# Kernel optimization log

Measured on AMD Instinct MI355X. Metric: run time of the kernel, lower is better.

The kernel has to match this reference:

```python
import jax, jax.numpy as jnp
from jax import lax
import numpy as np

NPOINT, RADIUS, NSAMPLE = 1024, 0.2, 32
MLP = [64, 64, 128]
IN_CH = 35  # 3 coord channels + 32 point features
EPS = 1e-5


def farthest_point_sample(xyz, npoint):
    # xyz: (B, N, 3) -> (B, npoint) int32. Deterministic start at index 0.
    B, N, _ = xyz.shape

    def step(carry, _):
        dist, farthest = carry  # (B,N), (B,)
        centroid = jnp.take_along_axis(xyz, farthest[:, None, None], axis=1)  # (B,1,3)
        d = jnp.sum((xyz - centroid) ** 2, axis=-1)  # (B,N)
        dist = jnp.minimum(dist, d)
        nxt = jnp.argmax(dist, axis=-1).astype(jnp.int32)
        return (dist, nxt), farthest

    init = (jnp.full((B, N), 1e10, xyz.dtype), jnp.zeros((B,), jnp.int32))
    _, idxs = lax.scan(step, init, None, length=npoint)
    return idxs.T  # (B, npoint)


def gather_points(points, idx):
    # points: (B, N, C); idx: (B, ...) int -> (B, ..., C)
    return jax.vmap(lambda p, i: p[i])(points, idx)


def query_ball_point(radius, nsample, xyz, new_xyz):
    # xyz: (B,N,3), new_xyz: (B,S,3) -> (B,S,nsample) int32
    B, N, _ = xyz.shape
    sqrdists = jnp.sum((new_xyz[:, :, None, :] - xyz[:, None, :, :]) ** 2, axis=-1)  # (B,S,N)
    group_idx = jnp.where(sqrdists > radius ** 2, N, jnp.arange(N, dtype=jnp.int32))
    group_idx = jnp.sort(group_idx, axis=-1)[:, :, :nsample]
    first = group_idx[:, :, :1]
    return jnp.where(group_idx == N, first, group_idx)


def sa_forward(xyz, points, params):
    B, N, C = xyz.shape
    fps_idx = farthest_point_sample(xyz, NPOINT)
    new_xyz = gather_points(xyz, fps_idx)  # (B,S,3)
    idx = query_ball_point(RADIUS, NSAMPLE, xyz, new_xyz)  # (B,S,K)
    grouped_xyz = gather_points(xyz, idx)  # (B,S,K,3)
    grouped_xyz_norm = grouped_xyz - new_xyz[:, :, None, :]
    grouped_points = gather_points(points, idx)  # (B,S,K,D)
    new_points = jnp.concatenate([grouped_xyz_norm, grouped_points], axis=-1)  # (B,S,K,Cin)
    x = new_points.transpose(0, 3, 2, 1)  # (B, Cin, K, S)
    for w, b, g, be in params:
        x = jnp.einsum('oi,biks->boks', w, x) + b[None, :, None, None]  # 1x1 conv
        mean = x.mean(axis=(0, 2, 3), keepdims=True)  # BatchNorm2d, training mode
        var = x.var(axis=(0, 2, 3), keepdims=True)
        x = (x - mean) / jnp.sqrt(var + EPS)
        x = jax.nn.relu(g[None, :, None, None] * x + be[None, :, None, None])
    new_points_out = x.max(axis=2)  # max over nsample -> (B, Cout, S)
    return new_xyz, new_points_out


def setup_inputs() -> dict:
    key = jax.random.key(0)
    ks = jax.random.split(key, 16)
    B, N, D = 16, 4096, 32
    inp = {
        'xyz': jax.random.uniform(ks[0], (B, N, 3), dtype=jnp.float32),
        'points': jax.random.normal(ks[1], (B, N, D), dtype=jnp.float32),
    }
    last = IN_CH
    for li, out_ch in enumerate(MLP):
        inp[f'w{li}'] = jax.random.normal(ks[2 + 4 * li], (out_ch, last), dtype=jnp.float32) * 0.05
        inp[f'b{li}'] = jnp.zeros((out_ch,), jnp.float32)
        inp[f'g{li}'] = jnp.ones((out_ch,), jnp.float32)
        inp[f'be{li}'] = jnp.zeros((out_ch,), jnp.float32)
        last = out_ch
    return inp


def reference(xyz, points, w0, b0, g0, be0, w1, b1, g1, be1, w2, b2, g2, be2):
    params = [(w0, b0, g0, be0), (w1, b1, g1, be1), (w2, b2, g2, be2)]
    return sa_forward(xyz, points, params)
```

## Files before the change

kernel.cpp:

```cpp
#include <hip/hip_runtime.h>
#include <stdint.h>

#pragma clang fp contract(off)

#define BATCH   16
#define NPTS    4096
#define NPOINT  1024
#define NSAMPLE 32
#define NPOS    (BATCH*NPOINT*NSAMPLE)
#define NBLK    (NPOS/128)
#define EPSV    1e-5f

typedef unsigned short ushort_t;
typedef unsigned int uint_t;
typedef unsigned long long u64;
typedef __attribute__((ext_vector_type(8))) short bf16x8;
typedef __attribute__((ext_vector_type(4))) float f32x4;
typedef __attribute__((ext_vector_type(2))) float f32x2;

__device__ inline ushort_t f2bf(float f) {
    uint_t u = __float_as_uint(f);
    u += 0x7fffu + ((u >> 16) & 1u);
    return (ushort_t)(u >> 16);
}
__device__ inline void unpack8(uint4 u, float* f) {
    f[0] = __uint_as_float(u.x << 16); f[1] = __uint_as_float(u.x & 0xffff0000u);
    f[2] = __uint_as_float(u.y << 16); f[3] = __uint_as_float(u.y & 0xffff0000u);
    f[4] = __uint_as_float(u.z << 16); f[5] = __uint_as_float(u.z & 0xffff0000u);
    f[6] = __uint_as_float(u.w << 16); f[7] = __uint_as_float(u.w & 0xffff0000u);
}

#define DPP_MAX_STAGE(CTRL) do {                                              \
    uint_t _lo2 = __builtin_amdgcn_update_dpp(lo, lo, CTRL, 0xf, 0xf, false); \
    uint_t _hi2 = __builtin_amdgcn_update_dpp(hi, hi, CTRL, 0xf, 0xf, false); \
    u64 _o = ((u64)_hi2 << 32) | _lo2;                                        \
    u64 _v = ((u64)hi << 32) | lo;                                            \
    bool _g = _o > _v;                                                        \
    lo = _g ? _lo2 : lo; hi = _g ? _hi2 : hi;                                 \
} while (0)

__global__ __launch_bounds__(512) void fps_kernel(const float* __restrict__ xyz,
                                                  float* __restrict__ new_xyz) {
    __shared__ float4 lxyz[NPTS];
    __shared__ u64 wbest[2][8];
    __shared__ int fpsidx[NPOINT];
    const int b = blockIdx.x;
    const int tid = threadIdx.x;
    const float* base = xyz + (size_t)b * NPTS * 3;
    for (int n = tid; n < NPTS; n += 512) {
        lxyz[n] = make_float4(base[3 * n], base[3 * n + 1], base[3 * n + 2], 0.f);
    }
    __syncthreads();

    f32x2 px[4], py[4], pz[4], dist[4];
    uint_t lowc[8];
#pragma unroll
    for (int j = 0; j < 4; j++) {
        float4 v0 = lxyz[tid + (2 * j) * 512];
        float4 v1 = lxyz[tid + (2 * j + 1) * 512];
        px[j] = (f32x2){v0.x, v1.x};
        py[j] = (f32x2){v0.y, v1.y};
        pz[j] = (f32x2){v0.z, v1.z};
        dist[j] = (f32x2){1e10f, 1e10f};
        lowc[2 * j] = ~(uint_t)(tid + (2 * j) * 512);
        lowc[2 * j + 1] = ~(uint_t)(tid + (2 * j + 1) * 512);
    }
    if (tid == 0) fpsidx[0] = 0;
    int cur = 0;
    const int lane = tid & 63, wid = tid >> 6;

    for (int it = 1; it < NPOINT; ++it) {
        float4 c = lxyz[cur];
        const f32x2 cx = (f32x2){c.x, c.x};
        const f32x2 cy = (f32x2){c.y, c.y};
        const f32x2 cz = (f32x2){c.z, c.z};
        u64 t[4];
#pragma unroll
        for (int j = 0; j < 4; j++) {
            f32x2 dx = px[j] - cx;
            f32x2 dy = py[j] - cy;
            f32x2 dz = pz[j] - cz;
            f32x2 d = (dx * dx + dy * dy) + dz * dz;
            f32x2 nd = __builtin_elementwise_min(dist[j], d);
            dist[j] = nd;
            u64 e0 = ((u64)__float_as_uint(nd.x) << 32) | lowc[2 * j];
            u64 e1 = ((u64)__float_as_uint(nd.y) << 32) | lowc[2 * j + 1];
            t[j] = e0 > e1 ? e0 : e1;
        }
        t[0] = t[0] > t[1] ? t[0] : t[1];
        t[2] = t[2] > t[3] ? t[2] : t[3];
        u64 v = t[0] > t[2] ? t[0] : t[2];

        uint_t lo = (uint_t)v, hi = (uint_t)(v >> 32);
        DPP_MAX_STAGE(0x111);
        DPP_MAX_STAGE(0x112);
        DPP_MAX_STAGE(0x114);
        DPP_MAX_STAGE(0x118);
        DPP_MAX_STAGE(0x142);
        DPP_MAX_STAGE(0x143);
        uint_t mlo = __builtin_amdgcn_readlane(lo, 63);
        uint_t mhi = __builtin_amdgcn_readlane(hi, 63);

        const int par = it & 1;
        if (lane == 0) wbest[par][wid] = ((u64)mhi << 32) | mlo;
        __syncthreads();
        u64 w0 = wbest[par][0], w1 = wbest[par][1];
        u64 w2 = wbest[par][2], w3 = wbest[par][3];
        u64 w4 = wbest[par][4], w5 = wbest[par][5];
        u64 w6 = wbest[par][6], w7 = wbest[par][7];
        u64 a0 = w0 > w1 ? w0 : w1;
        u64 a1 = w2 > w3 ? w2 : w3;
        u64 a2 = w4 > w5 ? w4 : w5;
        u64 a3 = w6 > w7 ? w6 : w7;
        a0 = a0 > a1 ? a0 : a1;
        a2 = a2 > a3 ? a2 : a3;
        u64 bb = a0 > a2 ? a0 : a2;
        cur = (int)(~(uint_t)bb) & (NPTS - 1);
        if (tid == 0) fpsidx[it] = cur;
    }
    __syncthreads();
    float* ob = new_xyz + (size_t)b * NPOINT * 3;
    for (int s = tid; s < NPOINT; s += 512) {
        float4 v = lxyz[fpsidx[s]];
        ob[3 * s + 0] = v.x; ob[3 * s + 1] = v.y; ob[3 * s + 2] = v.z;
    }
}

__global__ __launch_bounds__(256) void ballq_kernel(const float* __restrict__ xyz,
                                                    const float* __restrict__ new_xyz,
                                                    int* __restrict__ gidx) {
    const int gw = (int)((blockIdx.x * 256 + threadIdx.x) >> 6);
    const int lane = threadIdx.x & 63;
    const int b = gw / NPOINT, s = gw % NPOINT;
    const float* nb = new_xyz + ((size_t)b * NPOINT + s) * 3;
    const float cx = nb[0], cy = nb[1], cz = nb[2];
    const float* xb = xyz + (size_t)b * NPTS * 3;
    const float r2 = (float)(0.2 * 0.2);
    int cnt = 0;
    int first = -1;
    int* out = gidx + (size_t)gw * NSAMPLE;
    for (int j0 = 0; j0 < NPTS; j0 += 64) {
        int j = j0 + lane;
        float dx = __fsub_rn(xb[j * 3 + 0], cx);
        float dy = __fsub_rn(xb[j * 3 + 1], cy);
        float dz = __fsub_rn(xb[j * 3 + 2], cz);
        float d = __fadd_rn(__fadd_rn(__fmul_rn(dx, dx), __fmul_rn(dy, dy)),
                            __fmul_rn(dz, dz));
        bool pred = !(d > r2);
        u64 mask = __ballot(pred);
        if (first < 0 && mask != 0ull) first = j0 + (__ffsll((long long)mask) - 1);
        int before = __popcll(mask & ((1ull << lane) - 1ull));
        int slot = cnt + before;
        if (pred && slot < NSAMPLE) out[slot] = j;
        cnt += (int)__popcll(mask);
        if (cnt >= NSAMPLE) break;
    }
    if (cnt < NSAMPLE) {
        if (lane >= cnt && lane < NSAMPLE) out[lane] = first;
    }
}

__global__ __launch_bounds__(256) void conv1_mfma(const float* __restrict__ xyz,
                                                  const float* __restrict__ points,
                                                  const float* __restrict__ new_xyz,
                                                  const int* __restrict__ gidx,
                                                  const float* __restrict__ W,
                                                  const float* __restrict__ bias,
                                                  ushort_t* __restrict__ Y,
                                                  float* __restrict__ part_s,
                                                  float* __restrict__ part_q) {
    const int lane = threadIdx.x & 63, wid = threadIdx.x >> 6;
    const int l15 = lane & 15, quad = lane >> 4;
    const int p0 = blockIdx.x * 128 + wid * 32;

    bf16x8 Bp[4], Bx[4];
#pragma unroll
    for (int nt = 0; nt < 4; nt++) {
        const float* wr = W + (size_t)(nt * 16 + l15) * 35;
#pragma unroll
        for (int q = 0; q < 8; q++) Bp[nt][q] = (short)f2bf(wr[3 + quad * 8 + q]);
#pragma unroll
        for (int q = 0; q < 8; q++)
            Bx[nt][q] = (quad == 0 && q < 3) ? (short)f2bf(wr[q]) : (short)0;
    }
    f32x4 acc[2][4];
#pragma unroll
    for (int mt = 0; mt < 2; mt++)
#pragma unroll
        for (int nt = 0; nt < 4; nt++) acc[mt][nt] = (f32x4){0.f, 0.f, 0.f, 0.f};

#pragma unroll
    for (int mt = 0; mt < 2; mt++) {
        const int p = p0 + mt * 16 + l15;
        const int b = p >> 15, s = (p & 32767) >> 5;
        const int j = gidx[p];
        const float* pr = points + ((size_t)(b * NPTS + j)) * 32 + quad * 8;
        bf16x8 Ap, Ax;
#pragma unroll
        for (int q = 0; q < 8; q++) Ap[q] = (short)f2bf(pr[q]);
#pragma unroll
        for (int q = 0; q < 8; q++) Ax[q] = 0;
        const float* xp = xyz + ((size_t)(b * NPTS + j)) * 3;
        const float* nz = new_xyz + ((size_t)(b * NPOINT + s)) * 3;
        if (quad == 0) {
            Ax[0] = (short)f2bf(xp[0] - nz[0]);
            Ax[1] = (short)f2bf(xp[1] - nz[1]);
            Ax[2] = (short)f2bf(xp[2] - nz[2]);
        }
#pragma unroll
        for (int nt = 0; nt < 4; nt++) {
            acc[mt][nt] = __builtin_amdgcn_mfma_f32_16x16x32_bf16(Ap, Bp[nt], acc[mt][nt], 0, 0, 0);
            acc[mt][nt] = __builtin_amdgcn_mfma_f32_16x16x32_bf16(Ax, Bx[nt], acc[mt][nt], 0, 0, 0);
        }
    }
    float s_[4], q_[4];
#pragma unroll
    for (int nt = 0; nt < 4; nt++) { s_[nt] = 0.f; q_[nt] = 0.f; }
#pragma unroll
    for (int nt = 0; nt < 4; nt++) {
        const int ch = nt * 16 + l15;
        const float bs = bias[ch];
#pragma unroll
        for (int mt = 0; mt < 2; mt++) {
            const int pb = p0 + mt * 16 + quad * 4;
#pragma unroll
            for (int r = 0; r < 4; r++) {
                float x = acc[mt][nt][r] + bs;
                uint_t u = __float_as_uint(x);
                u += 0x7fffu + ((u >> 16) & 1u);
                Y[(size_t)(pb + r) * 64 + ch] = (ushort_t)(u >> 16);
                float v = __uint_as_float(u & 0xffff0000u);
                s_[nt] += v; q_[nt] += v * v;
            }
        }
    }
#pragma unroll
    for (int nt = 0; nt < 4; nt++) {
        s_[nt] += __shfl_xor(s_[nt], 16, 64); s_[nt] += __shfl_xor(s_[nt], 32, 64);
        q_[nt] += __shfl_xor(q_[nt], 16, 64); q_[nt] += __shfl_xor(q_[nt], 32, 64);
    }
    __shared__ float reds[4][4][16], redq[4][4][16];
    if (lane < 16) {
#pragma unroll
        for (int nt = 0; nt < 4; nt++) { reds[wid][nt][lane] = s_[nt]; redq[wid][nt][lane] = q_[nt]; }
    }
    __syncthreads();
    if (threadIdx.x < 16) {
#pragma unroll
        for (int nt = 0; nt < 4; nt++) {
            float ss = 0.f, qq = 0.f;
#pragma unroll
            for (int w = 0; w < 4; w++) { ss += reds[w][nt][threadIdx.x]; qq += redq[w][nt][threadIdx.x]; }
            const int ch = nt * 16 + threadIdx.x;
            part_s[(size_t)ch * NBLK + blockIdx.x] = ss;
            part_q[(size_t)ch * NBLK + blockIdx.x] = qq;
        }
    }
}

template <int IN, int OUT>
__global__ __launch_bounds__(256) void convN_mfma(const ushort_t* __restrict__ Yin,
                                                  const float* __restrict__ scale,
                                                  const float* __restrict__ shift,
                                                  const float* __restrict__ W,
                                                  const float* __restrict__ bias,
                                                  ushort_t* __restrict__ Yout,
                                                  float* __restrict__ part_s,
                                                  float* __restrict__ part_q) {
    constexpr int NT = OUT / 16;
    const int lane = threadIdx.x & 63, wid = threadIdx.x >> 6;
    const int l15 = lane & 15, quad = lane >> 4;
    const int p0 = blockIdx.x * 128 + wid * 32;

    float sc[2][8], sh[2][8];
#pragma unroll
    for (int kq = 0; kq < 2; kq++) {
        const int i0 = kq * 32 + quad * 8;
#pragma unroll
        for (int q = 0; q < 8; q++) { sc[kq][q] = scale[i0 + q]; sh[kq][q] = shift[i0 + q]; }
    }
    bf16x8 Bf[NT][2];
#pragma unroll
    for (int nt = 0; nt < NT; nt++)
#pragma unroll
        for (int kq = 0; kq < 2; kq++) {
            const float* wr = W + (size_t)(nt * 16 + l15) * IN + kq * 32 + quad * 8;
#pragma unroll
            for (int q = 0; q < 8; q++) Bf[nt][kq][q] = (short)f2bf(wr[q]);
        }

    bf16x8 Af[2][2];
#pragma unroll
    for (int mt = 0; mt < 2; mt++)
#pragma unroll
        for (int kq = 0; kq < 2; kq++) {
            const ushort_t* yr = Yin + (size_t)(p0 + mt * 16 + l15) * IN + kq * 32 + quad * 8;
            uint4 u = *(const uint4*)yr;
            float f[8]; unpack8(u, f);
#pragma unroll
            for (int q = 0; q < 8; q++) {
                float x = fmaxf(fmaf(f[q], sc[kq][q], sh[kq][q]), 0.f);
                Af[mt][kq][q] = (short)f2bf(x);
            }
        }

    f32x4 acc[2][NT];
#pragma unroll
    for (int mt = 0; mt < 2; mt++)
#pragma unroll
        for (int nt = 0; nt < NT; nt++) acc[mt][nt] = (f32x4){0.f, 0.f, 0.f, 0.f};
#pragma unroll
    for (int mt = 0; mt < 2; mt++)
#pragma unroll
        for (int nt = 0; nt < NT; nt++) {
            acc[mt][nt] = __builtin_amdgcn_mfma_f32_16x16x32_bf16(Af[mt][0], Bf[nt][0], acc[mt][nt], 0, 0, 0);
            acc[mt][nt] = __builtin_amdgcn_mfma_f32_16x16x32_bf16(Af[mt][1], Bf[nt][1], acc[mt][nt], 0, 0, 0);
        }
    float s_[NT], q_[NT];
#pragma unroll
    for (int nt = 0; nt < NT; nt++) { s_[nt] = 0.f; q_[nt] = 0.f; }
#pragma unroll
    for (int nt = 0; nt < NT; nt++) {
        const int ch = nt * 16 + l15;
        const float bs = bias[ch];
#pragma unroll
        for (int mt = 0; mt < 2; mt++) {
            const int pb = p0 + mt * 16 + quad * 4;
#pragma unroll
            for (int r = 0; r < 4; r++) {
                float x = acc[mt][nt][r] + bs;
                uint_t u = __float_as_uint(x);
                u += 0x7fffu + ((u >> 16) & 1u);
                Yout[(size_t)(pb + r) * OUT + ch] = (ushort_t)(u >> 16);
                float v = __uint_as_float(u & 0xffff0000u);
                s_[nt] += v; q_[nt] += v * v;
            }
        }
    }
#pragma unroll
    for (int nt = 0; nt < NT; nt++) {
        s_[nt] += __shfl_xor(s_[nt], 16, 64); s_[nt] += __shfl_xor(s_[nt], 32, 64);
        q_[nt] += __shfl_xor(q_[nt], 16, 64); q_[nt] += __shfl_xor(q_[nt], 32, 64);
    }
    __shared__ float reds[4][NT][16], redq[4][NT][16];
    if (lane < 16) {
#pragma unroll
        for (int nt = 0; nt < NT; nt++) { reds[wid][nt][lane] = s_[nt]; redq[wid][nt][lane] = q_[nt]; }
    }
    __syncthreads();
    if (threadIdx.x < 16) {
#pragma unroll
        for (int nt = 0; nt < NT; nt++) {
            float ss = 0.f, qq = 0.f;
#pragma unroll
            for (int w = 0; w < 4; w++) { ss += reds[w][nt][threadIdx.x]; qq += redq[w][nt][threadIdx.x]; }
            const int ch = nt * 16 + threadIdx.x;
            part_s[(size_t)ch * NBLK + blockIdx.x] = ss;
            part_q[(size_t)ch * NBLK + blockIdx.x] = qq;
        }
    }
}

__global__ __launch_bounds__(256) void reduce_finalize(const float* __restrict__ part_s,
                                                       const float* __restrict__ part_q,
                                                       const float* __restrict__ g,
                                                       const float* __restrict__ be,
                                                       float* __restrict__ scale,
                                                       float* __restrict__ shift) {
    const int ch = blockIdx.x;
    const float* p1 = part_s + (size_t)ch * NBLK;
    const float* p2 = part_q + (size_t)ch * NBLK;
    float s = 0.f, q = 0.f;
    for (int i = threadIdx.x; i < NBLK; i += 256) { s += p1[i]; q += p2[i]; }
#pragma unroll
    for (int m = 1; m < 64; m <<= 1) { s += __shfl_xor(s, m, 64); q += __shfl_xor(q, m, 64); }
    __shared__ float ls[4], lq[4];
    const int lane = threadIdx.x & 63, wid = threadIdx.x >> 6;
    if (lane == 0) { ls[wid] = s; lq[wid] = q; }
    __syncthreads();
    if (threadIdx.x == 0) {
        float ssum = ls[0] + ls[1] + ls[2] + ls[3];
        float qsum = lq[0] + lq[1] + lq[2] + lq[3];
        float mean = ssum * (1.f / (float)NPOS);
        float var = qsum * (1.f / (float)NPOS) - mean * mean;
        float inv = 1.f / sqrtf(var + EPSV);
        float sc = g[ch] * inv;
        scale[ch] = sc;
        shift[ch] = be[ch] - mean * sc;
    }
}

__global__ __launch_bounds__(256) void final_kernel(const ushort_t* __restrict__ Y3,
                                                    const float* __restrict__ scale,
                                                    const float* __restrict__ shift,
                                                    float* __restrict__ out) {
    const int b = blockIdx.x >> 5;
    const int stile = (blockIdx.x & 31) * 32;
    const int sl = threadIdx.x >> 3;
    const int oc = threadIdx.x & 7;
    const int s = stile + sl;
    const size_t base = ((size_t)(b * NPOINT + s)) * 32 * 128 + oc * 16;
    float vmax[16];
#pragma unroll
    for (int i = 0; i < 16; i++) vmax[i] = 0.f;
    for (int k = 0; k < 32; k++) {
        const ushort_t* yp = Y3 + base + (size_t)k * 128;
#pragma unroll
        for (int h = 0; h < 2; h++) {
            uint4 u = *(const uint4*)(yp + h * 8);
            float f[8];
            unpack8(u, f);
#pragma unroll
            for (int i = 0; i < 8; i++) {
                int o = oc * 16 + h * 8 + i;
                float v = fmaf(f[i], scale[o], shift[o]);
                vmax[h * 8 + i] = fmaxf(vmax[h * 8 + i], v);
            }
        }
    }
    __shared__ float res[32][130];
#pragma unroll
    for (int i = 0; i < 16; i++) res[sl][oc * 16 + i] = vmax[i];
    __syncthreads();
    const int so = threadIdx.x & 31;
    const int og = threadIdx.x >> 5;
#pragma unroll
    for (int r = 0; r < 16; r++) {
        int o = og * 16 + r;
        out[((size_t)(b * 128 + o)) * NPOINT + stile + so] = res[so][o];
    }
}

extern "C" void kernel_launch(void* const* d_in, const int* in_sizes, int n_in,
                              void* d_out, int out_size, void* d_ws, size_t ws_size,
                              hipStream_t stream) {
    const float* xyz = (const float*)d_in[0];
    const float* points = (const float*)d_in[1];
    const float* w0 = (const float*)d_in[2];
    const float* b0 = (const float*)d_in[3];
    const float* g0 = (const float*)d_in[4];
    const float* be0 = (const float*)d_in[5];
    const float* w1 = (const float*)d_in[6];
    const float* b1 = (const float*)d_in[7];
    const float* g1 = (const float*)d_in[8];
    const float* be1 = (const float*)d_in[9];
    const float* w2 = (const float*)d_in[10];
    const float* b2 = (const float*)d_in[11];
    const float* g2 = (const float*)d_in[12];
    const float* be2 = (const float*)d_in[13];

    float* out = (float*)d_out;
    float* new_xyz = out;
    float* final_out = out + BATCH * NPOINT * 3;

    char* ws = (char*)d_ws;
    const size_t MB = 1024u * 1024u;
    const size_t o_gidx = 0;
    const size_t o_y2 = 2 * MB;
    const size_t o_y13 = o_y2 + (size_t)NPOS * 64 * 2;
    const size_t o_params = o_y13 + (size_t)NPOS * 128 * 2;
    const size_t o_parts = o_params + 4096;

    int* gidx = (int*)(ws + o_gidx);
    ushort_t* Y1 = (ushort_t*)(ws + o_y13);
    ushort_t* Y2 = (ushort_t*)(ws + o_y2);
    ushort_t* Y3 = (ushort_t*)(ws + o_y13);
    float* pr = (float*)(ws + o_params);
    float* scale1 = pr + 0, *shift1 = pr + 64;
    float* scale2 = pr + 128, *shift2 = pr + 192;
    float* scale3 = pr + 256, *shift3 = pr + 384;
    float* part_s = (float*)(ws + o_parts);
    float* part_q = part_s + (size_t)128 * NBLK;

    fps_kernel<<<BATCH, 512, 0, stream>>>(xyz, new_xyz);
    ballq_kernel<<<(BATCH * NPOINT) / 4, 256, 0, stream>>>(xyz, new_xyz, gidx);
    conv1_mfma<<<NBLK, 256, 0, stream>>>(xyz, points, new_xyz, gidx, w0, b0, Y1, part_s, part_q);
    reduce_finalize<<<64, 256, 0, stream>>>(part_s, part_q, g0, be0, scale1, shift1);
    convN_mfma<64, 64><<<NBLK, 256, 0, stream>>>(Y1, scale1, shift1, w1, b1, Y2, part_s, part_q);
    reduce_finalize<<<64, 256, 0, stream>>>(part_s, part_q, g1, be1, scale2, shift2);
    convN_mfma<64, 128><<<NBLK, 256, 0, stream>>>(Y2, scale2, shift2, w2, b2, Y3, part_s, part_q);
    reduce_finalize<<<128, 256, 0, stream>>>(part_s, part_q, g2, be2, scale3, shift3);
    final_kernel<<<BATCH * 32, 256, 0, stream>>>(Y3, scale3, shift3, final_out);
}
```

Baseline: 1.048 ms.

## Pre-convert weights to bf16, halve FPS block size, pack bf16 conversions

A new prep kernel converts the conv weights to bf16 once per call, so each conv block loads them with vector loads instead of converting them itself. The FPS kernel drops from 512 to 256 threads per block, with each thread holding 16 points, which halves the cross-wave reduction at every iteration's barrier. Conv kernels switch to vector float4 loads and paired bf16 packing intrinsics for the activation conversion and the output epilogue. The costs are an extra kernel launch, more registers per FPS thread, and longer serial work per thread in FPS.

```diff
diff --git a/kernel.cpp b/kernel.cpp
--- a/kernel.cpp
+++ b/kernel.cpp
@@ -1,4 +1,5 @@
 #include <hip/hip_runtime.h>
+#include <hip/hip_bf16.h>
 #include <stdint.h>
 
 #pragma clang fp contract(off)
@@ -23,11 +24,33 @@
     u += 0x7fffu + ((u >> 16) & 1u);
     return (ushort_t)(u >> 16);
 }
+__device__ inline uint_t pkbf(float a, float b) {
+    __hip_bfloat162 h = __float22bfloat162_rn(make_float2(a, b));
+    uint_t r; __builtin_memcpy(&r, &h, 4); return r;
+}
+__device__ inline bf16x8 asbf(uint4 u) {
+    bf16x8 v; __builtin_memcpy(&v, &u, 16); return v;
+}
 __device__ inline void unpack8(uint4 u, float* f) {
     f[0] = __uint_as_float(u.x << 16); f[1] = __uint_as_float(u.x & 0xffff0000u);
     f[2] = __uint_as_float(u.y << 16); f[3] = __uint_as_float(u.y & 0xffff0000u);
     f[4] = __uint_as_float(u.z << 16); f[5] = __uint_as_float(u.z & 0xffff0000u);
     f[6] = __uint_as_float(u.w << 16); f[7] = __uint_as_float(u.w & 0xffff0000u);
+}
+
+__global__ __launch_bounds__(256) void prep_w(const float* __restrict__ w0,
+                                              const float* __restrict__ w1,
+                                              const float* __restrict__ w2,
+                                              ushort_t* __restrict__ Wp0,
+                                              ushort_t* __restrict__ Wx0,
+                                              ushort_t* __restrict__ Wp1,
+                                              ushort_t* __restrict__ Wp2) {
+    const int t = blockIdx.x * 256 + threadIdx.x;
+    const int stride = gridDim.x * 256;
+    for (int i = t; i < 64 * 32; i += stride) { int ch = i >> 5, k = i & 31; Wp0[i] = f2bf(w0[ch * 35 + 3 + k]); }
+    for (int i = t; i < 64 * 4;  i += stride) { int ch = i >> 2, q = i & 3;  Wx0[i] = (q < 3) ? f2bf(w0[ch * 35 + q]) : (ushort_t)0; }
+    for (int i = t; i < 64 * 64; i += stride) Wp1[i] = f2bf(w1[i]);
+    for (int i = t; i < 128 * 64; i += stride) Wp2[i] = f2bf(w2[i]);
 }
 
 #define DPP_MAX_STAGE(CTRL) do {                                              \
@@ -39,31 +62,31 @@
     lo = _g ? _lo2 : lo; hi = _g ? _hi2 : hi;                                 \
 } while (0)
 
-__global__ __launch_bounds__(512) void fps_kernel(const float* __restrict__ xyz,
+__global__ __launch_bounds__(256) void fps_kernel(const float* __restrict__ xyz,
                                                   float* __restrict__ new_xyz) {
     __shared__ float4 lxyz[NPTS];
-    __shared__ u64 wbest[2][8];
+    __shared__ u64 wbest[2][4];
     __shared__ int fpsidx[NPOINT];
     const int b = blockIdx.x;
     const int tid = threadIdx.x;
     const float* base = xyz + (size_t)b * NPTS * 3;
-    for (int n = tid; n < NPTS; n += 512) {
+    for (int n = tid; n < NPTS; n += 256) {
         lxyz[n] = make_float4(base[3 * n], base[3 * n + 1], base[3 * n + 2], 0.f);
     }
     __syncthreads();
 
-    f32x2 px[4], py[4], pz[4], dist[4];
-    uint_t lowc[8];
-#pragma unroll
-    for (int j = 0; j < 4; j++) {
-        float4 v0 = lxyz[tid + (2 * j) * 512];
-        float4 v1 = lxyz[tid + (2 * j + 1) * 512];
+    f32x2 px[8], py[8], pz[8], dist[8];
+    uint_t lowc[16];
+#pragma unroll
+    for (int j = 0; j < 8; j++) {
+        float4 v0 = lxyz[tid + (2 * j) * 256];
+        float4 v1 = lxyz[tid + (2 * j + 1) * 256];
         px[j] = (f32x2){v0.x, v1.x};
         py[j] = (f32x2){v0.y, v1.y};
         pz[j] = (f32x2){v0.z, v1.z};
         dist[j] = (f32x2){1e10f, 1e10f};
-        lowc[2 * j] = ~(uint_t)(tid + (2 * j) * 512);
-        lowc[2 * j + 1] = ~(uint_t)(tid + (2 * j + 1) * 512);
+        lowc[2 * j] = ~(uint_t)(tid + (2 * j) * 256);
+        lowc[2 * j + 1] = ~(uint_t)(tid + (2 * j + 1) * 256);
     }
     if (tid == 0) fpsidx[0] = 0;
     int cur = 0;
@@ -74,9 +97,9 @@
         const f32x2 cx = (f32x2){c.x, c.x};
         const f32x2 cy = (f32x2){c.y, c.y};
         const f32x2 cz = (f32x2){c.z, c.z};
-        u64 t[4];
-#pragma unroll
-        for (int j = 0; j < 4; j++) {
+        u64 t[8];
+#pragma unroll
+        for (int j = 0; j < 8; j++) {
             f32x2 dx = px[j] - cx;
             f32x2 dy = py[j] - cy;
             f32x2 dz = pz[j] - cz;
@@ -87,6 +110,8 @@
             u64 e1 = ((u64)__float_as_uint(nd.y) << 32) | lowc[2 * j + 1];
             t[j] = e0 > e1 ? e0 : e1;
         }
+#pragma unroll
+        for (int j = 0; j < 4; j++) { u64 o = t[j + 4]; t[j] = t[j] > o ? t[j] : o; }
         t[0] = t[0] > t[1] ? t[0] : t[1];
         t[2] = t[2] > t[3] ? t[2] : t[3];
         u64 v = t[0] > t[2] ? t[0] : t[2];
@@ -104,23 +129,17 @@
         const int par = it & 1;
         if (lane == 0) wbest[par][wid] = ((u64)mhi << 32) | mlo;
         __syncthreads();
-        u64 w0 = wbest[par][0], w1 = wbest[par][1];
-        u64 w2 = wbest[par][2], w3 = wbest[par][3];
-        u64 w4 = wbest[par][4], w5 = wbest[par][5];
-        u64 w6 = wbest[par][6], w7 = wbest[par][7];
-        u64 a0 = w0 > w1 ? w0 : w1;
-        u64 a1 = w2 > w3 ? w2 : w3;
-        u64 a2 = w4 > w5 ? w4 : w5;
-        u64 a3 = w6 > w7 ? w6 : w7;
-        a0 = a0 > a1 ? a0 : a1;
-        a2 = a2 > a3 ? a2 : a3;
-        u64 bb = a0 > a2 ? a0 : a2;
+        u64 b0 = wbest[par][0], b1 = wbest[par][1];
+        u64 b2 = wbest[par][2], b3 = wbest[par][3];
+        u64 m01 = b0 > b1 ? b0 : b1;
+        u64 m23 = b2 > b3 ? b2 : b3;
+        u64 bb = m01 > m23 ? m01 : m23;
         cur = (int)(~(uint_t)bb) & (NPTS - 1);
         if (tid == 0) fpsidx[it] = cur;
     }
     __syncthreads();
     float* ob = new_xyz + (size_t)b * NPOINT * 3;
-    for (int s = tid; s < NPOINT; s += 512) {
+    for (int s = tid; s < NPOINT; s += 256) {
         float4 v = lxyz[fpsidx[s]];
         ob[3 * s + 0] = v.x; ob[3 * s + 1] = v.y; ob[3 * s + 2] = v.z;
     }
@@ -164,7 +183,8 @@
                                                   const float* __restrict__ points,
                                                   const float* __restrict__ new_xyz,
                                                   const int* __restrict__ gidx,
-                                                  const float* __restrict__ W,
+                                                  const ushort_t* __restrict__ Wp0,
+                                                  const ushort_t* __restrict__ Wx0,
                                                   const float* __restrict__ bias,
                                                   ushort_t* __restrict__ Y,
                                                   float* __restrict__ part_s,
@@ -176,12 +196,14 @@
     bf16x8 Bp[4], Bx[4];
 #pragma unroll
     for (int nt = 0; nt < 4; nt++) {
-        const float* wr = W + (size_t)(nt * 16 + l15) * 35;
-#pragma unroll
-        for (int q = 0; q < 8; q++) Bp[nt][q] = (short)f2bf(wr[3 + quad * 8 + q]);
-#pragma unroll
-        for (int q = 0; q < 8; q++)
-            Bx[nt][q] = (quad == 0 && q < 3) ? (short)f2bf(wr[q]) : (short)0;
+        const int ch = nt * 16 + l15;
+        Bp[nt] = *(const bf16x8*)(Wp0 + (size_t)ch * 32 + quad * 8);
+        uint4 bx = {0u, 0u, 0u, 0u};
+        if (quad == 0) {
+            uint2 wv = *(const uint2*)(Wx0 + ch * 4);
+            bx.x = wv.x; bx.y = wv.y;
+        }
+        Bx[nt] = asbf(bx);
     }
     f32x4 acc[2][4];
 #pragma unroll
@@ -195,18 +217,21 @@
         const int b = p >> 15, s = (p & 32767) >> 5;
         const int j = gidx[p];
         const float* pr = points + ((size_t)(b * NPTS + j)) * 32 + quad * 8;
-        bf16x8 Ap, Ax;
-#pragma unroll
-        for (int q = 0; q < 8; q++) Ap[q] = (short)f2bf(pr[q]);
-#pragma unroll
-        for (int q = 0; q < 8; q++) Ax[q] = 0;
-        const float* xp = xyz + ((size_t)(b * NPTS + j)) * 3;
-        const float* nz = new_xyz + ((size_t)(b * NPOINT + s)) * 3;
+        float4 pa = *(const float4*)pr;
+        float4 pb4 = *(const float4*)(pr + 4);
+        uint4 ap;
+        ap.x = pkbf(pa.x, pa.y);  ap.y = pkbf(pa.z, pa.w);
+        ap.z = pkbf(pb4.x, pb4.y); ap.w = pkbf(pb4.z, pb4.w);
+        bf16x8 Ap = asbf(ap);
+        uint4 ax = {0u, 0u, 0u, 0u};
         if (quad == 0) {
-            Ax[0] = (short)f2bf(xp[0] - nz[0]);
-            Ax[1] = (short)f2bf(xp[1] - nz[1]);
-            Ax[2] = (short)f2bf(xp[2] - nz[2]);
-        }
+            const float* xp = xyz + ((size_t)(b * NPTS + j)) * 3;
+            const float* nz = new_xyz + ((size_t)(b * NPOINT + s)) * 3;
+            float d0 = xp[0] - nz[0], d1 = xp[1] - nz[1], d2 = xp[2] - nz[2];
+            ax.x = pkbf(d0, d1);
+            ax.y = pkbf(d2, 0.f);
+        }
+        bf16x8 Ax = asbf(ax);
 #pragma unroll
         for (int nt = 0; nt < 4; nt++) {
             acc[mt][nt] = __builtin_amdgcn_mfma_f32_16x16x32_bf16(Ap, Bp[nt], acc[mt][nt], 0, 0, 0);
@@ -223,15 +248,17 @@
 #pragma unroll
         for (int mt = 0; mt < 2; mt++) {
             const int pb = p0 + mt * 16 + quad * 4;
-#pragma unroll
-            for (int r = 0; r < 4; r++) {
-                float x = acc[mt][nt][r] + bs;
-                uint_t u = __float_as_uint(x);
-                u += 0x7fffu + ((u >> 16) & 1u);
-                Y[(size_t)(pb + r) * 64 + ch] = (ushort_t)(u >> 16);
-                float v = __uint_as_float(u & 0xffff0000u);
-                s_[nt] += v; q_[nt] += v * v;
-            }
+            float x0 = acc[mt][nt][0] + bs, x1 = acc[mt][nt][1] + bs;
+            float x2 = acc[mt][nt][2] + bs, x3 = acc[mt][nt][3] + bs;
+            uint_t p01 = pkbf(x0, x1), p23 = pkbf(x2, x3);
+            Y[(size_t)(pb + 0) * 64 + ch] = (ushort_t)(p01 & 0xffffu);
+            Y[(size_t)(pb + 1) * 64 + ch] = (ushort_t)(p01 >> 16);
+            Y[(size_t)(pb + 2) * 64 + ch] = (ushort_t)(p23 & 0xffffu);
+            Y[(size_t)(pb + 3) * 64 + ch] = (ushort_t)(p23 >> 16);
+            float v0 = __uint_as_float(p01 << 16), v1 = __uint_as_float(p01 & 0xffff0000u);
+            float v2 = __uint_as_float(p23 << 16), v3 = __uint_as_float(p23 & 0xffff0000u);
+            s_[nt] += (v0 + v1) + (v2 + v3);
+            q_[nt] += (v0 * v0 + v1 * v1) + (v2 * v2 + v3 * v3);
         }
     }
 #pragma unroll
@@ -262,7 +289,7 @@
 __global__ __launch_bounds__(256) void convN_mfma(const ushort_t* __restrict__ Yin,
                                                   const float* __restrict__ scale,
                                                   const float* __restrict__ shift,
-                                                  const float* __restrict__ W,
+                                                  const ushort_t* __restrict__ Wp,
                                                   const float* __restrict__ bias,
                                                   ushort_t* __restrict__ Yout,
                                                   float* __restrict__ part_s,
@@ -276,18 +303,21 @@
 #pragma unroll
     for (int kq = 0; kq < 2; kq++) {
         const int i0 = kq * 32 + quad * 8;
-#pragma unroll
-        for (int q = 0; q < 8; q++) { sc[kq][q] = scale[i0 + q]; sh[kq][q] = shift[i0 + q]; }
+        float4 a0 = *(const float4*)(scale + i0);
+        float4 a1 = *(const float4*)(scale + i0 + 4);
+        float4 b0v = *(const float4*)(shift + i0);
+        float4 b1v = *(const float4*)(shift + i0 + 4);
+        sc[kq][0] = a0.x; sc[kq][1] = a0.y; sc[kq][2] = a0.z; sc[kq][3] = a0.w;
+        sc[kq][4] = a1.x; sc[kq][5] = a1.y; sc[kq][6] = a1.z; sc[kq][7] = a1.w;
+        sh[kq][0] = b0v.x; sh[kq][1] = b0v.y; sh[kq][2] = b0v.z; sh[kq][3] = b0v.w;
+        sh[kq][4] = b1v.x; sh[kq][5] = b1v.y; sh[kq][6] = b1v.z; sh[kq][7] = b1v.w;
     }
     bf16x8 Bf[NT][2];
 #pragma unroll
     for (int nt = 0; nt < NT; nt++)
 #pragma unroll
-        for (int kq = 0; kq < 2; kq++) {
-            const float* wr = W + (size_t)(nt * 16 + l15) * IN + kq * 32 + quad * 8;
-#pragma unroll
-            for (int q = 0; q < 8; q++) Bf[nt][kq][q] = (short)f2bf(wr[q]);
-        }
+        for (int kq = 0; kq < 2; kq++)
+            Bf[nt][kq] = *(const bf16x8*)(Wp + (size_t)(nt * 16 + l15) * IN + kq * 32 + quad * 8);
 
     bf16x8 Af[2][2];
 #pragma unroll
@@ -297,11 +327,18 @@
             const ushort_t* yr = Yin + (size_t)(p0 + mt * 16 + l15) * IN + kq * 32 + quad * 8;
             uint4 u = *(const uint4*)yr;
             float f[8]; unpack8(u, f);
-#pragma unroll
-            for (int q = 0; q < 8; q++) {
-                float x = fmaxf(fmaf(f[q], sc[kq][q], sh[kq][q]), 0.f);
-                Af[mt][kq][q] = (short)f2bf(x);
-            }
+            float g0 = fmaxf(fmaf(f[0], sc[kq][0], sh[kq][0]), 0.f);
+            float g1 = fmaxf(fmaf(f[1], sc[kq][1], sh[kq][1]), 0.f);
+            float g2 = fmaxf(fmaf(f[2], sc[kq][2], sh[kq][2]), 0.f);
+            float g3 = fmaxf(fmaf(f[3], sc[kq][3], sh[kq][3]), 0.f);
+            float g4 = fmaxf(fmaf(f[4], sc[kq][4], sh[kq][4]), 0.f);
+            float g5 = fmaxf(fmaf(f[5], sc[kq][5], sh[kq][5]), 0.f);
+            float g6 = fmaxf(fmaf(f[6], sc[kq][6], sh[kq][6]), 0.f);
+            float g7 = fmaxf(fmaf(f[7], sc[kq][7], sh[kq][7]), 0.f);
+            uint4 a;
+            a.x = pkbf(g0, g1); a.y = pkbf(g2, g3);
+            a.z = pkbf(g4, g5); a.w = pkbf(g6, g7);
+            Af[mt][kq] = asbf(a);
         }
 
     f32x4 acc[2][NT];
@@ -326,15 +363,17 @@
 #pragma unroll
         for (int mt = 0; mt < 2; mt++) {
             const int pb = p0 + mt * 16 + quad * 4;
-#pragma unroll
-            for (int r = 0; r < 4; r++) {
-                float x = acc[mt][nt][r] + bs;
-                uint_t u = __float_as_uint(x);
-                u += 0x7fffu + ((u >> 16) & 1u);
-                Yout[(size_t)(pb + r) * OUT + ch] = (ushort_t)(u >> 16);
-                float v = __uint_as_float(u & 0xffff0000u);
-                s_[nt] += v; q_[nt] += v * v;
-            }
+            float x0 = acc[mt][nt][0] + bs, x1 = acc[mt][nt][1] + bs;
+            float x2 = acc[mt][nt][2] + bs, x3 = acc[mt][nt][3] + bs;
+            uint_t p01 = pkbf(x0, x1), p23 = pkbf(x2, x3);
+            Yout[(size_t)(pb + 0) * OUT + ch] = (ushort_t)(p01 & 0xffffu);
+            Yout[(size_t)(pb + 1) * OUT + ch] = (ushort_t)(p01 >> 16);
+            Yout[(size_t)(pb + 2) * OUT + ch] = (ushort_t)(p23 & 0xffffu);
+            Yout[(size_t)(pb + 3) * OUT + ch] = (ushort_t)(p23 >> 16);
+            float v0 = __uint_as_float(p01 << 16), v1 = __uint_as_float(p01 & 0xffff0000u);
+            float v2 = __uint_as_float(p23 << 16), v3 = __uint_as_float(p23 & 0xffff0000u);
+            s_[nt] += (v0 + v1) + (v2 + v3);
+            q_[nt] += (v0 * v0 + v1 * v1) + (v2 * v2 + v3 * v3);
         }
     }
 #pragma unroll
@@ -460,6 +499,7 @@
     const size_t o_y13 = o_y2 + (size_t)NPOS * 64 * 2;
     const size_t o_params = o_y13 + (size_t)NPOS * 128 * 2;
     const size_t o_parts = o_params + 4096;
+    const size_t o_w = o_parts + 4 * MB;
 
     int* gidx = (int*)(ws + o_gidx);
     ushort_t* Y1 = (ushort_t*)(ws + o_y13);
@@ -471,14 +511,19 @@
     float* scale3 = pr + 256, *shift3 = pr + 384;
     float* part_s = (float*)(ws + o_parts);
     float* part_q = part_s + (size_t)128 * NBLK;
-
-    fps_kernel<<<BATCH, 512, 0, stream>>>(xyz, new_xyz);
+    ushort_t* Wp0 = (ushort_t*)(ws + o_w);
+    ushort_t* Wx0 = Wp0 + 64 * 32;
+    ushort_t* Wp1 = Wx0 + 64 * 4;
+    ushort_t* Wp2 = Wp1 + 64 * 64;
+
+    prep_w<<<8, 256, 0, stream>>>(w0, w1, w2, Wp0, Wx0, Wp1, Wp2);
+    fps_kernel<<<BATCH, 256, 0, stream>>>(xyz, new_xyz);
     ballq_kernel<<<(BATCH * NPOINT) / 4, 256, 0, stream>>>(xyz, new_xyz, gidx);
-    conv1_mfma<<<NBLK, 256, 0, stream>>>(xyz, points, new_xyz, gidx, w0, b0, Y1, part_s, part_q);
+    conv1_mfma<<<NBLK, 256, 0, stream>>>(xyz, points, new_xyz, gidx, Wp0, Wx0, b0, Y1, part_s, part_q);
     reduce_finalize<<<64, 256, 0, stream>>>(part_s, part_q, g0, be0, scale1, shift1);
-    convN_mfma<64, 64><<<NBLK, 256, 0, stream>>>(Y1, scale1, shift1, w1, b1, Y2, part_s, part_q);
+    convN_mfma<64, 64><<<NBLK, 256, 0, stream>>>(Y1, scale1, shift1, Wp1, b1, Y2, part_s, part_q);
     reduce_finalize<<<64, 256, 0, stream>>>(part_s, part_q, g1, be1, scale2, shift2);
-    convN_mfma<64, 128><<<NBLK, 256, 0, stream>>>(Y2, scale2, shift2, w2, b2, Y3, part_s, part_q);
+    convN_mfma<64, 128><<<NBLK, 256, 0, stream>>>(Y2, scale2, shift2, Wp2, b2, Y3, part_s, part_q);
     reduce_finalize<<<128, 256, 0, stream>>>(part_s, part_q, g2, be2, scale3, shift3);
     final_kernel<<<BATCH * 32, 256, 0, stream>>>(Y3, scale3, shift3, final_out);
 }
```

New measurement: 909.6 us. 1.15x faster.
